# Kernel tuning notes

Hardware: AMD Instinct MI355X
Metric: run time of the kernel (lower is better)

Reference implementation:

```python
import jax, jax.numpy as jnp
import numpy as np

N, D, E, G, L = 65536, 512, 1048576, 128, 512


def setup_inputs() -> dict:
    key = jax.random.key(0)
    ks = jax.random.split(key, 12)
    s = 0.02
    # disjoint sequence groups: a permutation of all nodes reshaped to [G, L]
    seq_ids = jax.random.permutation(ks[0], N).reshape(G, L)
    return {
        'in_feats': jax.random.normal(ks[1], (N, D), jnp.float32),
        'edge_src': jax.random.randint(ks[2], (E,), 0, N),
        'edge_dst': jax.random.randint(ks[3], (E,), 0, N),
        'seq_ids': seq_ids,
        'W_conv': jax.random.normal(ks[4], (D, D), jnp.float32) * s,
        'b_conv': jnp.zeros((D,), jnp.float32),
        'W_ff1': jax.random.normal(ks[5], (D, D), jnp.float32) * s,
        'b_ff1': jnp.zeros((D,), jnp.float32),
        'W_ih': jax.random.normal(ks[6], (3 * D, D), jnp.float32) * s,
        'W_hh': jax.random.normal(ks[7], (3 * D, D), jnp.float32) * s,
        'b_ih': jnp.zeros((3 * D,), jnp.float32),
        'b_hh': jnp.zeros((3 * D,), jnp.float32),
        'W_ff2': jax.random.normal(ks[8], (D, D), jnp.float32) * s,
        'b_ff2': jnp.zeros((D,), jnp.float32),
    }


def _gru(x_lgd, W_ih, W_hh, b_ih, b_hh):
    # x_lgd: [L, G, D] (seq-major, batch_first=False); torch nn.GRU cell math
    d = W_hh.shape[1]
    # precompute input gates for all steps: [L, G, 3D]
    gi_all = jnp.einsum('lgd,ed->lge', x_lgd, W_ih) + b_ih

    def step(h, gi):
        gh = h @ W_hh.T + b_hh
        ir, iz, inn = jnp.split(gi, 3, axis=-1)
        hr, hz, hn = jnp.split(gh, 3, axis=-1)
        r = jax.nn.sigmoid(ir + hr)
        z = jax.nn.sigmoid(iz + hz)
        n = jnp.tanh(inn + r * hn)
        h_new = (1.0 - z) * n + z * h
        return h_new, h_new

    h0 = jnp.zeros((x_lgd.shape[1], d), x_lgd.dtype)
    _, ys = jax.lax.scan(step, h0, gi_all)
    return ys  # [L, G, D]


def reference(in_feats, edge_src, edge_dst, seq_ids, W_conv, b_conv,
              W_ff1, b_ff1, W_ih, W_hh, b_ih, b_hh, W_ff2, b_ff2):
    # conv_layer: mean aggregation over incoming edges, then Linear
    agg = jax.ops.segment_sum(in_feats[edge_src], edge_dst, num_segments=N)
    deg = jax.ops.segment_sum(jnp.ones((E,), in_feats.dtype), edge_dst, num_segments=N)
    agg = agg / jnp.maximum(deg, 1.0)[:, None]
    med = agg @ W_conv + b_conv                      # [N, D]
    # ff1
    med = jax.nn.relu(med @ W_ff1 + b_ff1)           # [N, D]
    # per-group seq_layer: gather [G, L, D], run GRU over L, scatter back
    seqs = med[seq_ids]                              # [G, L, D]
    ys = _gru(jnp.swapaxes(seqs, 0, 1), W_ih, W_hh, b_ih, b_hh)  # [L, G, D]
    ys = jnp.swapaxes(ys, 0, 1)                      # [G, L, D]
    # output[ids] += temp - output[ids]  ==  output[ids] = temp (disjoint ids)
    output = med.at[seq_ids.reshape(-1)].set(ys.reshape(-1, med.shape[-1]))
    # ff2
    return output @ W_ff2 + b_ff2
```

## Files before the change

### kernel.cpp

```cpp
#include <hip/hip_runtime.h>
#include <hip/hip_bf16.h>
#include <stdint.h>

typedef __hip_bfloat16 bf16;
typedef __attribute__((ext_vector_type(8))) short short8;
typedef __attribute__((ext_vector_type(4))) float f32x4;
typedef __attribute__((ext_vector_type(4))) unsigned int u32x4;

#define NN 65536
#define DD 512
#define EE 1048576
#define GG 128
#define LL 512

static __device__ __forceinline__ void gld_lds16(const void* g, void* l) {
  __builtin_amdgcn_global_load_lds((const __attribute__((address_space(1))) uint32_t*)g,
                                   (__attribute__((address_space(3))) uint32_t*)l, 16, 0, 0);
}

__global__ __launch_bounds__(256) void k_prep(
    const float* __restrict__ Wc, const float* __restrict__ Wf1, const float* __restrict__ Wf2,
    const float* __restrict__ Wih, const float* __restrict__ Whh,
    bf16* __restrict__ WcT, bf16* __restrict__ Wf1T, bf16* __restrict__ Wf2T,
    bf16* __restrict__ WihB, bf16* __restrict__ WhhB)
{
  const int i = blockIdx.x * 256 + threadIdx.x;
  if (i < 512 * 512) {
    const int k = i >> 9, n = i & 511;
    WcT [n * 512 + k] = __float2bfloat16(Wc [i]);
    Wf1T[n * 512 + k] = __float2bfloat16(Wf1[i]);
    Wf2T[n * 512 + k] = __float2bfloat16(Wf2[i]);
  }
  if (i < 1536 * 512) {
    WihB[i] = __float2bfloat16(Wih[i]);
    WhhB[i] = __float2bfloat16(Whh[i]);
  }
}

__global__ __launch_bounds__(256) void k_cast(const float* __restrict__ f, bf16* __restrict__ o) {
  const long i = (long)(blockIdx.x * 256 + threadIdx.x) * 4;
  const float4 v = *(const float4*)&f[i];
  union { bf16 b[4]; ushort4 u; } pk;
  pk.b[0] = __float2bfloat16(v.x);
  pk.b[1] = __float2bfloat16(v.y);
  pk.b[2] = __float2bfloat16(v.z);
  pk.b[3] = __float2bfloat16(v.w);
  *(ushort4*)&o[i] = pk.u;
}

__global__ __launch_bounds__(256) void k_deg(const int* __restrict__ dst, int* __restrict__ deg) {
  const int e = blockIdx.x * 256 + threadIdx.x;
  atomicAdd(&deg[dst[e]], 1);
}

__global__ __launch_bounds__(1024) void k_scan1(const int* __restrict__ deg,
                                                int* __restrict__ roff, int* __restrict__ partial) {
  __shared__ int sd[1024];
  const int t = threadIdx.x, b = blockIdx.x, i = b * 1024 + t;
  const int v = deg[i];
  sd[t] = v;
  __syncthreads();
  for (int off = 1; off < 1024; off <<= 1) {
    int add = (t >= off) ? sd[t - off] : 0;
    __syncthreads();
    sd[t] += add;
    __syncthreads();
  }
  roff[i] = sd[t] - v;
  if (t == 1023) partial[b] = sd[t];
}

__global__ __launch_bounds__(64) void k_scan2(const int* __restrict__ partial, int* __restrict__ base) {
  __shared__ int sd[64];
  const int t = threadIdx.x;
  const int v = partial[t];
  sd[t] = v;
  __syncthreads();
  for (int off = 1; off < 64; off <<= 1) {
    int add = (t >= off) ? sd[t - off] : 0;
    __syncthreads();
    sd[t] += add;
    __syncthreads();
  }
  base[t] = sd[t] - v;
  if (t == 63) base[64] = sd[63];
}

__global__ __launch_bounds__(1024) void k_scan3(const int* __restrict__ base,
                                                int* __restrict__ roff, int* __restrict__ cursor) {
  const int b = blockIdx.x, t = threadIdx.x, i = b * 1024 + t;
  const int v = roff[i] + base[b];
  roff[i] = v;
  cursor[i] = v;
  if (i == 0) roff[NN] = base[64];
}

__global__ __launch_bounds__(256) void k_fill(const int* __restrict__ src, const int* __restrict__ dst,
                                              int* __restrict__ cursor, int* __restrict__ csr) {
  const int e = blockIdx.x * 256 + threadIdx.x;
  const int p = atomicAdd(&cursor[dst[e]], 1);
  csr[p] = src[e];
}

__global__ __launch_bounds__(128) void k_agg(
    const bf16* __restrict__ featsb, const int* __restrict__ csr,
    const int* __restrict__ roff, bf16* __restrict__ agg)
{
  const int n = blockIdx.x, t = threadIdx.x;
  const int s0 = roff[n], s1 = roff[n + 1];
  float a0 = 0.f, a1 = 0.f, a2 = 0.f, a3 = 0.f;
  for (int i = s0; i < s1; ++i) {
    const int s = csr[i];
    const ushort4 v = *(const ushort4*)&featsb[(long)s * 512 + t * 4];
    bf16 b0, b1, b2, b3;
    *(uint16_t*)&b0 = v.x; *(uint16_t*)&b1 = v.y;
    *(uint16_t*)&b2 = v.z; *(uint16_t*)&b3 = v.w;
    a0 += __bfloat162float(b0); a1 += __bfloat162float(b1);
    a2 += __bfloat162float(b2); a3 += __bfloat162float(b3);
  }
  const float sc = 1.f / fmaxf((float)(s1 - s0), 1.f);
  union { bf16 b[4]; ushort4 u; } pk;
  pk.b[0] = __float2bfloat16(a0 * sc);
  pk.b[1] = __float2bfloat16(a1 * sc);
  pk.b[2] = __float2bfloat16(a2 * sc);
  pk.b[3] = __float2bfloat16(a3 * sc);
  *(ushort4*)&agg[(long)n * 512 + t * 4] = pk.u;
}

template<bool GATHER, bool RELU, bool SCATTER>
__global__ __launch_bounds__(256) void k_gemm(
    const bf16* __restrict__ A, const bf16* __restrict__ Bt,
    const float* __restrict__ bias, const int* __restrict__ gidx,
    bf16* __restrict__ outb, float* __restrict__ outf, int Ncols)
{
  __shared__ bf16 lsA[128 * 64];
  __shared__ bf16 lsB[128 * 64];
  const int t = threadIdx.x;
  const int lane = t & 63, wid = t >> 6;
  const int wr = wid >> 1, wc = wid & 1;
  const int tm = blockIdx.y * 128, tn = blockIdx.x * 128;
  const int col8 = (t & 7) * 8;
  const int rsub = t >> 3;
  const int lc = lane & 15, lk = lane >> 4;

  long arow[4], brow[4];
#pragma unroll
  for (int i = 0; i < 4; ++i) {
    const int r = tm + i * 32 + rsub;
    int ar = r;
    if constexpr (GATHER) ar = gidx[r];
    arow[i] = (long)ar * 512;
    brow[i] = (long)(tn + i * 32 + rsub) * 512;
  }

  f32x4 acc[4][4];
#pragma unroll
  for (int a = 0; a < 4; ++a)
#pragma unroll
    for (int b = 0; b < 4; ++b) acc[a][b] = (f32x4){0.f, 0.f, 0.f, 0.f};

  for (int ks = 0; ks < 8; ++ks) {
    const int k0 = ks * 64;
#pragma unroll
    for (int i = 0; i < 4; ++i) {
      gld_lds16(A  + arow[i] + k0 + col8, &lsA[i * 2048 + t * 8]);
      gld_lds16(Bt + brow[i] + k0 + col8, &lsB[i * 2048 + t * 8]);
    }
    __syncthreads();
#pragma unroll
    for (int kk = 0; kk < 2; ++kk) {
      short8 af[4], bfr[4];
#pragma unroll
      for (int mi = 0; mi < 4; ++mi)
        af[mi] = *(const short8*)&lsA[(wr * 64 + mi * 16 + lc) * 64 + kk * 32 + lk * 8];
#pragma unroll
      for (int ni = 0; ni < 4; ++ni)
        bfr[ni] = *(const short8*)&lsB[(wc * 64 + ni * 16 + lc) * 64 + kk * 32 + lk * 8];
#pragma unroll
      for (int mi = 0; mi < 4; ++mi)
#pragma unroll
        for (int ni = 0; ni < 4; ++ni)
          acc[mi][ni] = __builtin_amdgcn_mfma_f32_16x16x32_bf16(af[mi], bfr[ni], acc[mi][ni], 0, 0, 0);
    }
    __syncthreads();
  }

  float bv[4];
#pragma unroll
  for (int ni = 0; ni < 4; ++ni) bv[ni] = bias[tn + wc * 64 + ni * 16 + lc];

#pragma unroll
  for (int mi = 0; mi < 4; ++mi) {
    const int r0 = tm + wr * 64 + mi * 16 + lk * 4;
#pragma unroll
    for (int j = 0; j < 4; ++j) {
      const int row = r0 + j;
      long orow;
      if constexpr (SCATTER) orow = (long)gidx[row] * 512;
      else                   orow = (long)row * Ncols;
#pragma unroll
      for (int ni = 0; ni < 4; ++ni) {
        float v = acc[mi][ni][j] + bv[ni];
        if constexpr (RELU) v = fmaxf(v, 0.f);
        const int c = tn + wc * 64 + ni * 16 + lc;
        if constexpr (SCATTER) outf[orow + c] = v;
        else                   outb[orow + c] = __float2bfloat16(v);
      }
    }
  }
}

__global__ __launch_bounds__(128, 1) void k_gru5(
    const bf16* __restrict__ Whh, const float* __restrict__ bhh,
    const bf16* __restrict__ gi, bf16* __restrict__ hx,
    bf16* __restrict__ ys, int* __restrict__ flags)
{
  __shared__ bf16 lsW[96 * 520];
  const int t = threadIdx.x, lane = t & 63, w = t >> 6;
  const int chain = blockIdx.x >> 4, jcb = blockIdx.x & 15;
  const int lc = lane & 15, lk = lane >> 4;
  const int g0 = chain * 16;
  const int cols0 = jcb * 32;
  const int d = cols0 + w * 16 + lc;

#pragma unroll
  for (int it = 0; it < 48; ++it) {
    const int c = it * 128 + t;
    const int row = c >> 6, col8 = (c & 63) * 8;
    const int e = ((row >> 5) << 9) + cols0 + (row & 31);
    *(uint4*)&lsW[row * 520 + col8] = *(const uint4*)&Whh[(long)e * 512 + col8];
  }
  __syncthreads();

  const float bR = bhh[d], bZ = bhh[512 + d], bN = bhh[1024 + d];
  float hreg[4] = {0.f, 0.f, 0.f, 0.f};

  const bf16* pb0 = hx + chain * 8192 + lc * 512 + lk * 8;
  const bf16* gp[4];
  long ysb4[4];
  int hsb[4];
#pragma unroll
  for (int j = 0; j < 4; ++j) {
    const int gl = lk * 4 + j;
    const int g = g0 + gl;
    gp[j]   = gi + (long)g * 786432 + d;
    ysb4[j] = ((long)g << 18) + d;
    hsb[j]  = chain * 8192 + gl * 512 + d;
  }
  int* chflags = flags + chain * 32;
  int* myflag  = chflags + jcb * 2 + w;

  for (int l = 0; l < 512; ++l) {
    uint32_t gr[12];
#pragma unroll
    for (int j = 0; j < 4; ++j) {
      asm volatile("global_load_ushort %0, %1, off"             : "=v"(gr[j * 3 + 0]) : "v"(gp[j]) : "memory");
      asm volatile("global_load_ushort %0, %1, off offset:1024" : "=v"(gr[j * 3 + 1]) : "v"(gp[j]) : "memory");
      asm volatile("global_load_ushort %0, %1, off offset:2048" : "=v"(gr[j * 3 + 2]) : "v"(gp[j]) : "memory");
      gp[j] += 1536;
    }

    f32x4 acc[3] = { (f32x4){0.f,0.f,0.f,0.f}, (f32x4){0.f,0.f,0.f,0.f}, (f32x4){0.f,0.f,0.f,0.f} };
    if (l > 0) {
      int ok;
      do {
        const int v = __hip_atomic_load(&chflags[lane & 31], __ATOMIC_RELAXED,
                                        __HIP_MEMORY_SCOPE_AGENT);
        ok = __all(v >= l);
      } while (!ok);
      asm volatile("" ::: "memory");

      const bf16* pb = pb0 + (((l - 1) & 1) << 16);
      u32x4 hv[16];
#pragma unroll
      for (int kk = 0; kk < 16; ++kk)
        asm volatile("global_load_dwordx4 %0, %1, off offset:%2 sc0 sc1"
                     : "=v"(hv[kk]) : "v"(pb), "n"(kk * 64) : "memory");
      asm volatile("s_waitcnt vmcnt(0)" ::: "memory");
      __builtin_amdgcn_sched_barrier(0);

#pragma unroll
      for (int kk = 0; kk < 16; ++kk) {
        union { u32x4 u; short8 s; } cv;
        cv.u = hv[kk];
#pragma unroll
        for (int gate = 0; gate < 3; ++gate) {
          const short8 bfr = *(const short8*)&lsW[(gate * 32 + w * 16 + lc) * 520 + kk * 32 + lk * 8];
          acc[gate] = __builtin_amdgcn_mfma_f32_16x16x32_bf16(cv.s, bfr, acc[gate], 0, 0, 0);
        }
      }
    } else {
      asm volatile("s_waitcnt vmcnt(0)" ::: "memory");
      __builtin_amdgcn_sched_barrier(0);
    }

    bf16* hw = hx + ((l & 1) << 16);
    uint32_t hbits[4];
#pragma unroll
    for (int j = 0; j < 4; ++j) {
      union { uint32_t u; float f; } cu;
      cu.u = gr[j * 3 + 0] << 16;  const float giR = cu.f;
      cu.u = gr[j * 3 + 1] << 16;  const float giZ = cu.f;
      cu.u = gr[j * 3 + 2] << 16;  const float giN = cu.f;
      const float r = 1.f / (1.f + __expf(-(giR + acc[0][j] + bR)));
      const float z = 1.f / (1.f + __expf(-(giZ + acc[1][j] + bZ)));
      const float x2 = giN + r * (acc[2][j] + bN);
      const float ex = __expf(2.f * x2);
      const float n = 1.f - 2.f / (ex + 1.f);
      const float hn = (1.f - z) * n + z * hreg[j];
      hreg[j] = hn;
      const bf16 hnb = __float2bfloat16(hn);
      hbits[j] = (uint32_t)(*(const uint16_t*)&hnb);
      asm volatile("global_store_short %0, %1, off sc0 sc1"
                   :: "v"(hw + hsb[j]), "v"(hbits[j]) : "memory");
    }
#pragma unroll
    for (int j = 0; j < 4; ++j)
      asm volatile("global_store_short %0, %1, off nt"
                   :: "v"(ys + ysb4[j] + ((long)l << 9)), "v"(hbits[j]) : "memory");
    asm volatile("s_waitcnt vmcnt(4)" ::: "memory");
    if (lane == 0)
      __hip_atomic_store(myflag, l + 1, __ATOMIC_RELAXED, __HIP_MEMORY_SCOPE_AGENT);
  }
}

extern "C" void kernel_launch(void* const* d_in, const int* in_sizes, int n_in,
                              void* d_out, int out_size, void* d_ws, size_t ws_size,
                              hipStream_t stream)
{
  (void)in_sizes; (void)n_in; (void)out_size; (void)ws_size;
  const float* in_feats = (const float*)d_in[0];
  const int*   e_src    = (const int*)d_in[1];
  const int*   e_dst    = (const int*)d_in[2];
  const int*   seq      = (const int*)d_in[3];
  const float* W_conv   = (const float*)d_in[4];
  const float* b_conv   = (const float*)d_in[5];
  const float* W_ff1    = (const float*)d_in[6];
  const float* b_ff1    = (const float*)d_in[7];
  const float* W_ih     = (const float*)d_in[8];
  const float* W_hh     = (const float*)d_in[9];
  const float* b_ih     = (const float*)d_in[10];
  const float* b_hh     = (const float*)d_in[11];
  const float* W_ff2    = (const float*)d_in[12];
  const float* b_ff2    = (const float*)d_in[13];

  uint8_t* ws = (uint8_t*)d_ws;
  int*  deg     = (int*) (ws + 0);
  int*  cursor  = (int*) (ws + 262144u);
  int*  roff    = (int*) (ws + 524288u);
  bf16* WcT     = (bf16*)(ws + 1048576u);
  bf16* Wf1T    = (bf16*)(ws + 1572864u);
  bf16* Wf2T    = (bf16*)(ws + 2097152u);
  bf16* WihB    = (bf16*)(ws + 2621440u);
  bf16* WhhB    = (bf16*)(ws + 4194304u);
  int*  csr     = (int*) (ws + 6291456u);
  int*  flags   = (int*) (ws + 10485760u);
  int*  partial = (int*) (ws + 10616832u);
  int*  sbase   = (int*) (ws + 10620928u);
  bf16* hx      = (bf16*)(ws + 11534336u);
  bf16* med2    = (bf16*)(ws + 16777216u);
  bf16* ysb     = med2;
  bf16* gib     = (bf16*)(ws + 83886080u);
  bf16* aggb    = (bf16*)(ws + 83886080u);
  bf16* med1    = (bf16*)(ws + 150994944u);
  bf16* featsb  = (bf16*)(ws + 150994944u);

  hipMemsetAsync(deg,   0, NN * 4,     stream);
  hipMemsetAsync(flags, 0, 8 * 32 * 4, stream);

  k_prep <<<3072, 256, 0, stream>>>(W_conv, W_ff1, W_ff2, W_ih, W_hh, WcT, Wf1T, Wf2T, WihB, WhhB);
  k_cast <<<NN * DD / 1024, 256, 0, stream>>>(in_feats, featsb);
  k_deg  <<<EE / 256, 256, 0, stream>>>(e_dst, deg);
  k_scan1<<<64, 1024, 0, stream>>>(deg, roff, partial);
  k_scan2<<<1, 64, 0, stream>>>(partial, sbase);
  k_scan3<<<64, 1024, 0, stream>>>(sbase, roff, cursor);
  k_fill <<<EE / 256, 256, 0, stream>>>(e_src, e_dst, cursor, csr);
  k_agg  <<<NN, 128, 0, stream>>>(featsb, csr, roff, aggb);

  dim3 g512(4, 512), g1536(12, 512);
  k_gemm<false, false, false><<<g512,  256, 0, stream>>>(aggb, WcT,  b_conv, nullptr, med1, nullptr, 512);
  k_gemm<false, true,  false><<<g512,  256, 0, stream>>>(med1, Wf1T, b_ff1,  nullptr, med2, nullptr, 512);
  k_gemm<true,  false, false><<<g1536, 256, 0, stream>>>(med2, WihB, b_ih,   seq,     gib,  nullptr, 1536);

  k_gru5<<<128, 128, 0, stream>>>(WhhB, b_hh, gib, hx, ysb, flags);

  k_gemm<false, false, true><<<g512, 256, 0, stream>>>(ysb, Wf2T, b_ff2, seq, nullptr, (float*)d_out, 512);
}
```

Baseline: 3.008 ms.

## Transpose GRU MFMA to vectorize gate loads and write h directly into ys

The GRU recurrence swaps the MFMA operand order so each lane owns 4 consecutive hidden columns of one group. That lets it load the input gates with dwordx2 and store h with a single packed dwordx2 instead of many ushort accesses. The ping-pong hx buffer is dropped; each step writes h once into a per-step tiled ys buffer that the next step reads back. A new ff2 GEMM reads this tiled layout and scatters to the output. This removes the duplicate h store and cuts the number of per-step memory instructions on the latency-bound serial path, at the cost of a full vmcnt(0) wait before each flag publish.

Result: faster. 2.540 ms (-15.6%).

```diff
diff --git a/kernel.cpp b/kernel.cpp
--- a/kernel.cpp
+++ b/kernel.cpp
@@ -6,6 +6,7 @@
 typedef __attribute__((ext_vector_type(8))) short short8;
 typedef __attribute__((ext_vector_type(4))) float f32x4;
 typedef __attribute__((ext_vector_type(4))) unsigned int u32x4;
+typedef __attribute__((ext_vector_type(2))) unsigned int u32x2;
 
 #define NN 65536
 #define DD 512
@@ -127,11 +128,11 @@
   *(ushort4*)&agg[(long)n * 512 + t * 4] = pk.u;
 }
 
-template<bool GATHER, bool RELU, bool SCATTER>
+template<bool GATHER, bool RELU>
 __global__ __launch_bounds__(256) void k_gemm(
     const bf16* __restrict__ A, const bf16* __restrict__ Bt,
     const float* __restrict__ bias, const int* __restrict__ gidx,
-    bf16* __restrict__ outb, float* __restrict__ outf, int Ncols)
+    bf16* __restrict__ outb, int Ncols)
 {
   __shared__ bf16 lsA[128 * 64];
   __shared__ bf16 lsB[128 * 64];
@@ -195,25 +196,99 @@
 #pragma unroll
     for (int j = 0; j < 4; ++j) {
       const int row = r0 + j;
-      long orow;
-      if constexpr (SCATTER) orow = (long)gidx[row] * 512;
-      else                   orow = (long)row * Ncols;
+      const long orow = (long)row * Ncols;
 #pragma unroll
       for (int ni = 0; ni < 4; ++ni) {
         float v = acc[mi][ni][j] + bv[ni];
         if constexpr (RELU) v = fmaxf(v, 0.f);
         const int c = tn + wc * 64 + ni * 16 + lc;
-        if constexpr (SCATTER) outf[orow + c] = v;
-        else                   outb[orow + c] = __float2bfloat16(v);
+        outb[orow + c] = __float2bfloat16(v);
       }
     }
   }
 }
 
-__global__ __launch_bounds__(128, 1) void k_gru5(
+__global__ __launch_bounds__(256) void k_gemm_ys(
+    const uint8_t* __restrict__ Ay, const bf16* __restrict__ Bt,
+    const float* __restrict__ bias, const int* __restrict__ gidx,
+    float* __restrict__ outf)
+{
+  __shared__ bf16 lsA[128 * 64];
+  __shared__ bf16 lsB[128 * 64];
+  const int t = threadIdx.x;
+  const int lane = t & 63, wid = t >> 6;
+  const int wr = wid >> 1, wc = wid & 1;
+  const int tm = blockIdx.y * 128, tn = blockIdx.x * 128;
+  const int col8 = (t & 7) * 8;
+  const int rsub = t >> 3;
+  const int lc = lane & 15, lk = lane >> 4;
+
+  long arow[4], brow[4];
+#pragma unroll
+  for (int i = 0; i < 4; ++i) {
+    const int r = tm + i * 32 + rsub;
+    const int g = r >> 9, l = r & 511;
+    arow[i] = ((long)l * 8 + (g >> 4)) * 16384 + (g & 15) * 32;
+    brow[i] = (long)(tn + i * 32 + rsub) * 512;
+  }
+
+  f32x4 acc[4][4];
+#pragma unroll
+  for (int a = 0; a < 4; ++a)
+#pragma unroll
+    for (int b = 0; b < 4; ++b) acc[a][b] = (f32x4){0.f, 0.f, 0.f, 0.f};
+
+  for (int ks = 0; ks < 8; ++ks) {
+    const int k0 = ks * 64;
+    const int kk16 = k0 + col8;
+    const long aoff = ((long)(kk16 >> 4) << 9) + ((kk16 & 15) << 1);
+#pragma unroll
+    for (int i = 0; i < 4; ++i) {
+      gld_lds16(Ay + arow[i] + aoff, &lsA[i * 2048 + t * 8]);
+      gld_lds16(Bt + brow[i] + k0 + col8, &lsB[i * 2048 + t * 8]);
+    }
+    __syncthreads();
+#pragma unroll
+    for (int kk = 0; kk < 2; ++kk) {
+      short8 af[4], bfr[4];
+#pragma unroll
+      for (int mi = 0; mi < 4; ++mi)
+        af[mi] = *(const short8*)&lsA[(wr * 64 + mi * 16 + lc) * 64 + kk * 32 + lk * 8];
+#pragma unroll
+      for (int ni = 0; ni < 4; ++ni)
+        bfr[ni] = *(const short8*)&lsB[(wc * 64 + ni * 16 + lc) * 64 + kk * 32 + lk * 8];
+#pragma unroll
+      for (int mi = 0; mi < 4; ++mi)
+#pragma unroll
+        for (int ni = 0; ni < 4; ++ni)
+          acc[mi][ni] = __builtin_amdgcn_mfma_f32_16x16x32_bf16(af[mi], bfr[ni], acc[mi][ni], 0, 0, 0);
+    }
+    __syncthreads();
+  }
+
+  float bv[4];
+#pragma unroll
+  for (int ni = 0; ni < 4; ++ni) bv[ni] = bias[tn + wc * 64 + ni * 16 + lc];
+
+#pragma unroll
+  for (int mi = 0; mi < 4; ++mi) {
+    const int r0 = tm + wr * 64 + mi * 16 + lk * 4;
+#pragma unroll
+    for (int j = 0; j < 4; ++j) {
+      const int row = r0 + j;
+      const long orow = (long)gidx[row] * 512;
+#pragma unroll
+      for (int ni = 0; ni < 4; ++ni) {
+        const int c = tn + wc * 64 + ni * 16 + lc;
+        outf[orow + c] = acc[mi][ni][j] + bv[ni];
+      }
+    }
+  }
+}
+
+__global__ __launch_bounds__(128, 1) void k_gru7(
     const bf16* __restrict__ Whh, const float* __restrict__ bhh,
-    const bf16* __restrict__ gi, bf16* __restrict__ hx,
-    bf16* __restrict__ ys, int* __restrict__ flags)
+    const bf16* __restrict__ gi, uint8_t* __restrict__ ys2, int* __restrict__ flags)
 {
   __shared__ bf16 lsW[96 * 520];
   const int t = threadIdx.x, lane = t & 63, w = t >> 6;
@@ -221,7 +296,8 @@
   const int lc = lane & 15, lk = lane >> 4;
   const int g0 = chain * 16;
   const int cols0 = jcb * 32;
-  const int d = cols0 + w * 16 + lc;
+  const int p = jcb * 2 + w;
+  const int d0 = p * 16 + lk * 4;
 
 #pragma unroll
   for (int it = 0; it < 48; ++it) {
@@ -232,33 +308,28 @@
   }
   __syncthreads();
 
-  const float bR = bhh[d], bZ = bhh[512 + d], bN = bhh[1024 + d];
+  float bRa[4], bZa[4], bNa[4];
+#pragma unroll
+  for (int j = 0; j < 4; ++j) {
+    bRa[j] = bhh[d0 + j];
+    bZa[j] = bhh[512 + d0 + j];
+    bNa[j] = bhh[1024 + d0 + j];
+  }
   float hreg[4] = {0.f, 0.f, 0.f, 0.f};
 
-  const bf16* pb0 = hx + chain * 8192 + lc * 512 + lk * 8;
-  const bf16* gp[4];
-  long ysb4[4];
-  int hsb[4];
-#pragma unroll
-  for (int j = 0; j < 4; ++j) {
-    const int gl = lk * 4 + j;
-    const int g = g0 + gl;
-    gp[j]   = gi + (long)g * 786432 + d;
-    ysb4[j] = ((long)g << 18) + d;
-    hsb[j]  = chain * 8192 + gl * 512 + d;
-  }
+  const bf16* gp = gi + (long)(g0 + lc) * 786432 + d0;
+  uint8_t* psto = ys2 + (long)chain * 16384 + p * 512 + lc * 32 + lk * 8;
+  const long laneoff = (long)(lk >> 1) * 512 + lc * 32 + (lk & 1) * 16;
+
   int* chflags = flags + chain * 32;
-  int* myflag  = chflags + jcb * 2 + w;
+  int* myflag  = chflags + p;
 
   for (int l = 0; l < 512; ++l) {
-    uint32_t gr[12];
-#pragma unroll
-    for (int j = 0; j < 4; ++j) {
-      asm volatile("global_load_ushort %0, %1, off"             : "=v"(gr[j * 3 + 0]) : "v"(gp[j]) : "memory");
-      asm volatile("global_load_ushort %0, %1, off offset:1024" : "=v"(gr[j * 3 + 1]) : "v"(gp[j]) : "memory");
-      asm volatile("global_load_ushort %0, %1, off offset:2048" : "=v"(gr[j * 3 + 2]) : "v"(gp[j]) : "memory");
-      gp[j] += 1536;
-    }
+    u32x2 gRv, gZv, gNv;
+    asm volatile("global_load_dwordx2 %0, %1, off"             : "=v"(gRv) : "v"(gp) : "memory");
+    asm volatile("global_load_dwordx2 %0, %1, off offset:1024" : "=v"(gZv) : "v"(gp) : "memory");
+    asm volatile("global_load_dwordx2 %0, %1, off offset:2048" : "=v"(gNv) : "v"(gp) : "memory");
+    gp += 1536;
 
     f32x4 acc[3] = { (f32x4){0.f,0.f,0.f,0.f}, (f32x4){0.f,0.f,0.f,0.f}, (f32x4){0.f,0.f,0.f,0.f} };
     if (l > 0) {
@@ -270,12 +341,16 @@
       } while (!ok);
       asm volatile("" ::: "memory");
 
-      const bf16* pb = pb0 + (((l - 1) & 1) << 16);
+      const uint8_t* pb = ys2 + ((long)(l - 1) * 8 + chain) * 16384 + laneoff;
       u32x4 hv[16];
 #pragma unroll
-      for (int kk = 0; kk < 16; ++kk)
-        asm volatile("global_load_dwordx4 %0, %1, off offset:%2 sc0 sc1"
-                     : "=v"(hv[kk]) : "v"(pb), "n"(kk * 64) : "memory");
+      for (int q = 0; q < 4; ++q) {
+        const uint8_t* pbq = pb + q * 4096;
+#pragma unroll
+        for (int r2 = 0; r2 < 4; ++r2)
+          asm volatile("global_load_dwordx4 %0, %1, off offset:%2 sc0 sc1"
+                       : "=v"(hv[q * 4 + r2]) : "v"(pbq), "n"(r2 * 1024) : "memory");
+      }
       asm volatile("s_waitcnt vmcnt(0)" ::: "memory");
       __builtin_amdgcn_sched_barrier(0);
 
@@ -285,8 +360,8 @@
         cv.u = hv[kk];
 #pragma unroll
         for (int gate = 0; gate < 3; ++gate) {
-          const short8 bfr = *(const short8*)&lsW[(gate * 32 + w * 16 + lc) * 520 + kk * 32 + lk * 8];
-          acc[gate] = __builtin_amdgcn_mfma_f32_16x16x32_bf16(cv.s, bfr, acc[gate], 0, 0, 0);
+          const short8 wfr = *(const short8*)&lsW[(gate * 32 + w * 16 + lc) * 520 + kk * 32 + lk * 8];
+          acc[gate] = __builtin_amdgcn_mfma_f32_16x16x32_bf16(wfr, cv.s, acc[gate], 0, 0, 0);
         }
       }
     } else {
@@ -294,31 +369,30 @@
       __builtin_amdgcn_sched_barrier(0);
     }
 
-    bf16* hw = hx + ((l & 1) << 16);
-    uint32_t hbits[4];
+    uint32_t hb[4];
 #pragma unroll
     for (int j = 0; j < 4; ++j) {
-      union { uint32_t u; float f; } cu;
-      cu.u = gr[j * 3 + 0] << 16;  const float giR = cu.f;
-      cu.u = gr[j * 3 + 1] << 16;  const float giZ = cu.f;
-      cu.u = gr[j * 3 + 2] << 16;  const float giN = cu.f;
-      const float r = 1.f / (1.f + __expf(-(giR + acc[0][j] + bR)));
-      const float z = 1.f / (1.f + __expf(-(giZ + acc[1][j] + bZ)));
-      const float x2 = giN + r * (acc[2][j] + bN);
+      const uint32_t sh = (j & 1) * 16;
+      union { uint32_t u; float f; } cR, cZ, cN;
+      cR.u = ((gRv[j >> 1] >> sh) & 0xffffu) << 16;
+      cZ.u = ((gZv[j >> 1] >> sh) & 0xffffu) << 16;
+      cN.u = ((gNv[j >> 1] >> sh) & 0xffffu) << 16;
+      const float r = 1.f / (1.f + __expf(-(cR.f + acc[0][j] + bRa[j])));
+      const float z = 1.f / (1.f + __expf(-(cZ.f + acc[1][j] + bZa[j])));
+      const float x2 = cN.f + r * (acc[2][j] + bNa[j]);
       const float ex = __expf(2.f * x2);
       const float n = 1.f - 2.f / (ex + 1.f);
       const float hn = (1.f - z) * n + z * hreg[j];
       hreg[j] = hn;
       const bf16 hnb = __float2bfloat16(hn);
-      hbits[j] = (uint32_t)(*(const uint16_t*)&hnb);
-      asm volatile("global_store_short %0, %1, off sc0 sc1"
-                   :: "v"(hw + hsb[j]), "v"(hbits[j]) : "memory");
-    }
-#pragma unroll
-    for (int j = 0; j < 4; ++j)
-      asm volatile("global_store_short %0, %1, off nt"
-                   :: "v"(ys + ysb4[j] + ((long)l << 9)), "v"(hbits[j]) : "memory");
-    asm volatile("s_waitcnt vmcnt(4)" ::: "memory");
+      hb[j] = (uint32_t)(*(const uint16_t*)&hnb);
+    }
+    u32x2 hp;
+    hp[0] = hb[0] | (hb[1] << 16);
+    hp[1] = hb[2] | (hb[3] << 16);
+    asm volatile("global_store_dwordx2 %0, %1, off sc0 sc1" :: "v"(psto), "v"(hp) : "memory");
+    psto += 131072;
+    asm volatile("s_waitcnt vmcnt(0)" ::: "memory");
     if (lane == 0)
       __hip_atomic_store(myflag, l + 1, __ATOMIC_RELAXED, __HIP_MEMORY_SCOPE_AGENT);
   }
@@ -357,9 +431,8 @@
   int*  flags   = (int*) (ws + 10485760u);
   int*  partial = (int*) (ws + 10616832u);
   int*  sbase   = (int*) (ws + 10620928u);
-  bf16* hx      = (bf16*)(ws + 11534336u);
   bf16* med2    = (bf16*)(ws + 16777216u);
-  bf16* ysb     = med2;
+  uint8_t* ys2  = (uint8_t*)med2;
   bf16* gib     = (bf16*)(ws + 83886080u);
   bf16* aggb    = (bf16*)(ws + 83886080u);
   bf16* med1    = (bf16*)(ws + 150994944u);
@@ -378,11 +451,11 @@
   k_agg  <<<NN, 128, 0, stream>>>(featsb, csr, roff, aggb);
 
   dim3 g512(4, 512), g1536(12, 512);
-  k_gemm<false, false, false><<<g512,  256, 0, stream>>>(aggb, WcT,  b_conv, nullptr, med1, nullptr, 512);
-  k_gemm<false, true,  false><<<g512,  256, 0, stream>>>(med1, Wf1T, b_ff1,  nullptr, med2, nullptr, 512);
-  k_gemm<true,  false, false><<<g1536, 256, 0, stream>>>(med2, WihB, b_ih,   seq,     gib,  nullptr, 1536);
-
-  k_gru5<<<128, 128, 0, stream>>>(WhhB, b_hh, gib, hx, ysb, flags);
-
-  k_gemm<false, false, true><<<g512, 256, 0, stream>>>(ysb, Wf2T, b_ff2, seq, nullptr, (float*)d_out, 512);
-}
+  k_gemm<false, false><<<g512,  256, 0, stream>>>(aggb, WcT,  b_conv, nullptr, med1, 512);
+  k_gemm<false, true ><<<g512,  256, 0, stream>>>(med1, Wf1T, b_ff1,  nullptr, med2, 512);
+  k_gemm<true,  false><<<g1536, 256, 0, stream>>>(med2, WihB, b_ih,   seq,     gib,  1536);
+
+  k_gru7<<<128, 128, 0, stream>>>(WhhB, b_hh, gib, ys2, flags);
+
+  k_gemm_ys<<<g512, 256, 0, stream>>>(ys2, Wf2T, b_ff2, seq, (float*)d_out);
+}
```
